# Kernel tuning notes

Hardware: AMD Instinct MI355X
Metric: run time of the kernel (lower is better)

## Reference

```python
import jax, jax.numpy as jnp
import numpy as np

B, N, D = 4, 4096, 768
K_TOP = 8  # module's self.k
EPS = 1e-12  # F.normalize eps


def setup_inputs() -> dict:
    key = jax.random.key(0)
    k0, k1, k2 = jax.random.split(key, 3)
    s = 1.0 / np.sqrt(D)
    feats = jax.random.normal(k0, (B, N, D), dtype=jnp.float32)
    Wq = jax.random.normal(k1, (D, D), dtype=jnp.float32) * s
    bq = jnp.zeros((D,), dtype=jnp.float32)
    Wkv = jax.random.normal(k2, (D, 2 * D), dtype=jnp.float32) * s
    bkv = jnp.zeros((2 * D,), dtype=jnp.float32)
    return {"feats": feats, "Wq": Wq, "bq": bq, "Wkv": Wkv, "bkv": bkv}


def _l2norm(x):
    return x / jnp.maximum(jnp.linalg.norm(x, axis=-1, keepdims=True), EPS)


def reference(feats, Wq, bq, Wkv, bkv):
    # Only self.q and self.kv are used in the original forward; the
    # transformer encoder / norm / score_head / proj are dead code there.
    b, n, d = feats.shape
    Q = feats @ Wq + bq                      # [B,N,D]
    KV = feats @ Wkv + bkv                   # [B,N,2D]
    Kmat, Vmat = jnp.split(KV, 2, axis=-1)   # [B,N,D] each

    # cosine-distance kNN graph (self excluded via +1e6 on diagonal)
    sim = jnp.einsum('bnd,bmd->bnm', _l2norm(Q), _l2norm(Kmat))
    dist = (1.0 - sim) + jnp.eye(n, dtype=sim.dtype)[None] * 1e6
    k_eff = min(n - 1, K_TOP)
    _, idx = jax.lax.top_k(-dist, k_eff)     # smallest distances -> [B,N,k]

    # gather neighbor K/V (no O(N^2 * D) expand)
    bidx = jnp.arange(b)[:, None, None]
    Kn = Kmat[bidx, idx]                     # [B,N,k,D]
    Vn = Vmat[bidx, idx]                     # [B,N,k,D]

    attn = jnp.einsum('bnd,bnkd->bnk', Q, Kn) / np.float32(np.sqrt(d))
    attn = jax.nn.softmax(attn, axis=-1)     # [B,N,k]
    out = jnp.einsum('bnk,bnkd->bnd', attn, Vn)
    return out.mean(axis=1)                  # [B,D]
```

## Files before the change

### kernel.cpp

```cpp
#include <hip/hip_runtime.h>
#include <hip/hip_bf16.h>
#include <math.h>

#define B_ 4
#define N_ 4096
#define D_ 768
#define KTOP 8
#define M_ (B_*N_)
#define TCAND 12
#define KSPLIT 16
#define QBK 32

typedef __attribute__((ext_vector_type(8))) short short8;
typedef __attribute__((ext_vector_type(4))) float f32x4;
typedef _Float16 half_t;
typedef __attribute__((ext_vector_type(8))) _Float16 half8;
typedef __attribute__((ext_vector_type(4))) _Float16 half4;

__device__ __forceinline__ ushort f2bf(float f) {
    unsigned int u = __float_as_uint(f);
    unsigned int r = (u + 0x7FFFu + ((u >> 16) & 1u)) >> 16;
    return (ushort)r;
}

__device__ __forceinline__ void gload16(const void* g, void* l) {
    __builtin_amdgcn_global_load_lds(
        (const __attribute__((address_space(1))) unsigned int*)g,
        (__attribute__((address_space(3))) unsigned int*)l, 16, 0, 0);
}

__global__ __launch_bounds__(256) void split_feats(
    const float* __restrict__ f, half_t* __restrict__ Fh, half_t* __restrict__ Fl)
{
    const int i = (blockIdx.x * 256 + threadIdx.x) * 4;
    const float4 v = *(const float4*)&f[i];
    float x[4] = {v.x, v.y, v.z, v.w};
    half4 h, l;
#pragma unroll
    for (int c = 0; c < 4; ++c) {
        const half_t hh = (half_t)x[c];
        h[c] = hh;
        l[c] = (half_t)(x[c] - (float)hh);
    }
    *(half4*)&Fh[i] = h;
    *(half4*)&Fl[i] = l;
}

__global__ __launch_bounds__(256) void split_w(
    const float* __restrict__ Wq, const float* __restrict__ Wkv,
    half_t* __restrict__ Wth, half_t* __restrict__ Wtl)
{
    __shared__ float T[64][65];
    const int tid = threadIdx.x;
    const int n0 = blockIdx.x * 64;
    const int k0 = blockIdx.y * 64;

    const int nl = tid & 63;
#pragma unroll
    for (int r = 0; r < 16; ++r) {
        const int kl = (tid >> 6) * 16 + r;
        const int n  = n0 + nl;
        const float w = (n < 768)
            ? Wq[(size_t)(k0 + kl) * 768 + n]
            : Wkv[(size_t)(k0 + kl) * 1536 + (n - 768)];
        T[kl][nl] = w;
    }
    __syncthreads();

    const int kl2 = tid & 63;
#pragma unroll
    for (int r = 0; r < 16; ++r) {
        const int nl2 = (tid >> 6) * 16 + r;
        const float ws = T[kl2][nl2] * 4096.0f;
        const half_t h = (half_t)ws;
        const half_t l = (half_t)(ws - (float)h);
        Wth[(size_t)(n0 + nl2) * D_ + k0 + kl2] = h;
        Wtl[(size_t)(n0 + nl2) * D_ + k0 + kl2] = l;
    }
}

__global__ __launch_bounds__(256) void qkv_mfma(
    const half_t* __restrict__ Fh, const half_t* __restrict__ Fl,
    const half_t* __restrict__ Wth, const half_t* __restrict__ Wtl,
    const float* __restrict__ bq, const float* __restrict__ bkv,
    float* __restrict__ Q, float* __restrict__ Km, float* __restrict__ Vm)
{
    __shared__ __align__(16) half_t Ah[128 * QBK];
    __shared__ __align__(16) half_t Al[128 * QBK];
    __shared__ __align__(16) half_t Bh[128 * QBK];
    __shared__ __align__(16) half_t Bl[128 * QBK];

    const int tid  = threadIdx.x;
    const int lane = tid & 63, w = tid >> 6;
    const int wr = w >> 1, wc = w & 1;
    const int r16 = lane & 15, kq = lane >> 4;
    const int n0 = blockIdx.x * 128;
    const int m0 = blockIdx.y * 128;
    const bool three = (n0 < 1536);

    const half_t* ah = Fh  + (size_t)(m0 + (tid >> 2)) * D_ + (tid & 3) * 8;
    const half_t* al = Fl  + (size_t)(m0 + (tid >> 2)) * D_ + (tid & 3) * 8;
    const half_t* bh = Wth + (size_t)(n0 + (tid >> 2)) * D_ + (tid & 3) * 8;
    const half_t* bl = Wtl + (size_t)(n0 + (tid >> 2)) * D_ + (tid & 3) * 8;
    half_t* lAh = Ah + (w << 9);
    half_t* lAl = Al + (w << 9);
    half_t* lBh = Bh + (w << 9);
    half_t* lBl = Bl + (w << 9);

    f32x4 acc[4][4];
#pragma unroll
    for (int mi = 0; mi < 4; ++mi)
#pragma unroll
        for (int ni = 0; ni < 4; ++ni) acc[mi][ni] = (f32x4)0.f;

    for (int kb = 0; kb < D_ / QBK; ++kb) {
#pragma unroll
        for (int i = 0; i < 2; ++i) {
            gload16(ah + (size_t)i * 64 * D_ + kb * QBK, lAh + i * 2048);
            gload16(bh + (size_t)i * 64 * D_ + kb * QBK, lBh + i * 2048);
        }
        if (three) {
#pragma unroll
            for (int i = 0; i < 2; ++i) {
                gload16(al + (size_t)i * 64 * D_ + kb * QBK, lAl + i * 2048);
                gload16(bl + (size_t)i * 64 * D_ + kb * QBK, lBl + i * 2048);
            }
        }
        __syncthreads();
        {
            half8 fa[4], fb[4];
#pragma unroll
            for (int mi = 0; mi < 4; ++mi)
                fa[mi] = *(const half8*)&Ah[(wr * 64 + mi * 16 + r16) * QBK + kq * 8];
#pragma unroll
            for (int ni = 0; ni < 4; ++ni)
                fb[ni] = *(const half8*)&Bh[(wc * 64 + ni * 16 + r16) * QBK + kq * 8];
#pragma unroll
            for (int mi = 0; mi < 4; ++mi)
#pragma unroll
                for (int ni = 0; ni < 4; ++ni)
                    acc[mi][ni] = __builtin_amdgcn_mfma_f32_16x16x32_f16(
                        fa[mi], fb[ni], acc[mi][ni], 0, 0, 0);
            if (three) {
                half8 gal[4], gbl[4];
#pragma unroll
                for (int mi = 0; mi < 4; ++mi)
                    gal[mi] = *(const half8*)&Al[(wr * 64 + mi * 16 + r16) * QBK + kq * 8];
#pragma unroll
                for (int ni = 0; ni < 4; ++ni)
                    gbl[ni] = *(const half8*)&Bl[(wc * 64 + ni * 16 + r16) * QBK + kq * 8];
#pragma unroll
                for (int mi = 0; mi < 4; ++mi)
#pragma unroll
                    for (int ni = 0; ni < 4; ++ni) {
                        acc[mi][ni] = __builtin_amdgcn_mfma_f32_16x16x32_f16(
                            fa[mi], gbl[ni], acc[mi][ni], 0, 0, 0);
                        acc[mi][ni] = __builtin_amdgcn_mfma_f32_16x16x32_f16(
                            gal[mi], fb[ni], acc[mi][ni], 0, 0, 0);
                    }
            }
        }
        __syncthreads();
    }

    const float unscale = 1.0f / 4096.0f;
#pragma unroll
    for (int ni = 0; ni < 4; ++ni) {
        const int n = n0 + wc * 64 + ni * 16 + r16;
        const float bias = (n0 < 768) ? bq[n] : bkv[n - 768];
        float* dst; int nn;
        if      (n0 < 768)  { dst = Q;  nn = n; }
        else if (n0 < 1536) { dst = Km; nn = n - 768; }
        else                { dst = Vm; nn = n - 1536; }
#pragma unroll
        for (int mi = 0; mi < 4; ++mi)
#pragma unroll
            for (int r = 0; r < 4; ++r) {
                const int m = m0 + wr * 64 + mi * 16 + kq * 4 + r;
                dst[(size_t)m * D_ + nn] = acc[mi][ni][r] * unscale + bias;
            }
    }
}

__global__ __launch_bounds__(256) void norm_bf16(
    const float* __restrict__ Q, const float* __restrict__ Km,
    ushort* __restrict__ qn, ushort* __restrict__ kn,
    float* __restrict__ rqinv, float* __restrict__ rkinv)
{
    const int wid  = blockIdx.x * 4 + (threadIdx.x >> 6);
    const int lane = threadIdx.x & 63;
    const float* src; ushort* dst; float* rv; int r;
    if (wid < M_) { src = Q;  dst = qn; rv = rqinv; r = wid; }
    else          { src = Km; dst = kn; rv = rkinv; r = wid - M_; }
    const float* p = src + (size_t)r * D_ + lane * 12;
    float v[12];
#pragma unroll
    for (int i = 0; i < 3; ++i) *(float4*)&v[i * 4] = *(const float4*)&p[i * 4];
    float s = 0.f;
#pragma unroll
    for (int i = 0; i < 12; ++i) s += v[i] * v[i];
#pragma unroll
    for (int off = 32; off; off >>= 1) s += __shfl_xor(s, off);
    const float rinv = 1.0f / fmaxf(sqrtf(s), 1e-12f);
    ushort* op = dst + (size_t)r * D_ + lane * 12;
#pragma unroll
    for (int i = 0; i < 3; ++i) {
        ushort4 o;
        o.x = f2bf(v[i * 4 + 0] * rinv); o.y = f2bf(v[i * 4 + 1] * rinv);
        o.z = f2bf(v[i * 4 + 2] * rinv); o.w = f2bf(v[i * 4 + 3] * rinv);
        *(ushort4*)&op[i * 4] = o;
    }
    if (lane == 0) rv[r] = rinv;
}

__global__ __launch_bounds__(256) void sim_gemm(
    const ushort* __restrict__ qn, const ushort* __restrict__ kn,
    ushort* __restrict__ S)
{
    __shared__ __align__(16) ushort As[128 * 64];
    __shared__ __align__(16) ushort Bs[128 * 64];

    const int tid  = threadIdx.x;
    const int lane = tid & 63, w = tid >> 6;
    const int wr = w >> 1, wc = w & 1;
    const int r16 = lane & 15, kq = lane >> 4;
    const int k0 = blockIdx.x * 128;
    const int q0 = blockIdx.y * 128;

    const ushort* qsrc = qn + (size_t)(q0 + (tid >> 3)) * D_ + (tid & 7) * 8;
    const ushort* ksrc = kn + (size_t)(k0 + (tid >> 3)) * D_ + (tid & 7) * 8;
    ushort* lA = As + ((tid >> 6) << 9);
    ushort* lB = Bs + ((tid >> 6) << 9);

    f32x4 acc[4][4];
#pragma unroll
    for (int mi = 0; mi < 4; ++mi)
#pragma unroll
        for (int ni = 0; ni < 4; ++ni) acc[mi][ni] = (f32x4)0.f;

    for (int kb = 0; kb < D_ / 64; ++kb) {
#pragma unroll
        for (int i = 0; i < 4; ++i) {
            gload16(qsrc + (size_t)i * 32 * D_ + kb * 64, lA + i * 2048);
            gload16(ksrc + (size_t)i * 32 * D_ + kb * 64, lB + i * 2048);
        }
        __syncthreads();
#pragma unroll
        for (int kk = 0; kk < 2; ++kk) {
            short8 a[4], bfr[4];
#pragma unroll
            for (int mi = 0; mi < 4; ++mi)
                a[mi] = *(const short8*)&As[(wr * 64 + mi * 16 + r16) * 64 + kk * 32 + kq * 8];
#pragma unroll
            for (int ni = 0; ni < 4; ++ni)
                bfr[ni] = *(const short8*)&Bs[(wc * 64 + ni * 16 + r16) * 64 + kk * 32 + kq * 8];
#pragma unroll
            for (int mi = 0; mi < 4; ++mi)
#pragma unroll
                for (int ni = 0; ni < 4; ++ni)
                    acc[mi][ni] = __builtin_amdgcn_mfma_f32_16x16x32_bf16(
                        a[mi], bfr[ni], acc[mi][ni], 0, 0, 0);
        }
        __syncthreads();
    }

#pragma unroll
    for (int mi = 0; mi < 4; ++mi)
#pragma unroll
        for (int ni = 0; ni < 4; ++ni)
#pragma unroll
            for (int r = 0; r < 4; ++r) {
                const int qq = q0 + wr * 64 + mi * 16 + kq * 4 + r;
                const int kk = k0 + wc * 64 + ni * 16 + r16;
                const float val = acc[mi][ni][r];
                const ushort bv = (qq == kk) ? (ushort)0xFF7Fu : f2bf(val);
                S[(size_t)qq * N_ + kk] = bv;
            }
}

__global__ __launch_bounds__(256) void sel_topk(
    const ushort* __restrict__ S, unsigned int* __restrict__ Part)
{
    const int tid = threadIdx.x;
    const int row = blockIdx.x * 256 + tid;
    const int ks  = blockIdx.y;
    const int kbase = ks * 256;
    const int KREV  = (N_ - 1) - kbase;

    const ushort* sp = S + (size_t)row * N_ + kbase;
    unsigned int t[TCAND];
#pragma unroll
    for (int i = 0; i < TCAND; ++i) t[i] = 0u;

    for (int j = 0; j < 256; j += 8) {
        const uint4 dv = *(const uint4*)(sp + j);
        unsigned int dw[4];
        dw[0] = dv.x; dw[1] = dv.y; dw[2] = dv.z; dw[3] = dv.w;
#pragma unroll
        for (int q = 0; q < 4; ++q) {
            const unsigned int vlo = dw[q] & 0xFFFFu;
            const unsigned int vhi = dw[q] >> 16;
            const unsigned int plo =
                ((vlo ^ (0x8000u + ((vlo >> 15) * 0x7FFFu))) << 16) |
                (unsigned int)(KREV - (j + 2 * q));
            const unsigned int phi =
                ((vhi ^ (0x8000u + ((vhi >> 15) * 0x7FFFu))) << 16) |
                (unsigned int)(KREV - (j + 2 * q + 1));
            unsigned int p = plo;
#pragma unroll
            for (int i = 0; i < TCAND; ++i) {
                const unsigned int mx = max(t[i], p);
                const unsigned int mn = min(t[i], p);
                t[i] = mx; p = mn;
            }
            p = phi;
#pragma unroll
            for (int i = 0; i < TCAND; ++i) {
                const unsigned int mx = max(t[i], p);
                const unsigned int mn = min(t[i], p);
                t[i] = mx; p = mn;
            }
        }
    }

    unsigned int* op = Part + (size_t)row * (KSPLIT * TCAND) + ks * TCAND;
#pragma unroll
    for (int i = 0; i < TCAND; ++i) op[i] = t[i];
}

__global__ void zero_out(float* __restrict__ out)
{
    const int i = blockIdx.x * 256 + threadIdx.x;
    if (i < B_ * D_) out[i] = 0.f;
}

__global__ __launch_bounds__(256) void merge_rescore_attn(
    const float* __restrict__ Q, const float* __restrict__ Kmat,
    const float* __restrict__ Vmat, const float* __restrict__ rqinv,
    const float* __restrict__ rkinv, const unsigned int* __restrict__ Part,
    float* __restrict__ out)
{
    __shared__ float laccum[4][D_];
    const int tid  = threadIdx.x;
    const int w    = tid >> 6, lane = tid & 63;
    const int row  = blockIdx.x * 4 + w;
    const int b    = row >> 12;

    const unsigned int* pp = Part + (size_t)row * (KSPLIT * TCAND);
    unsigned int c0 = pp[lane], c1 = pp[64 + lane], c2 = pp[128 + lane];
    unsigned int mysel = 0u;
#pragma unroll
    for (int it = 0; it < TCAND; ++it) {
        unsigned int m = max(c0, max(c1, c2));
#pragma unroll
        for (int off = 32; off; off >>= 1) m = max(m, __shfl_xor(m, off));
        c0 = (c0 == m) ? 0u : c0;
        c1 = (c1 == m) ? 0u : c1;
        c2 = (c2 == m) ? 0u : c2;
        mysel = (lane == it) ? m : mysel;
    }
    const int kj_lane = (N_ - 1) - (int)(mysel & 0xFFFFu);

    int ka[TCAND];
#pragma unroll
    for (int j = 0; j < TCAND; ++j) ka[j] = __shfl(kj_lane, j);

    float qv[12];
    {
        const float* qp = Q + (size_t)row * D_ + lane * 12;
#pragma unroll
        for (int i = 0; i < 3; ++i) *(float4*)&qv[i * 4] = *(const float4*)&qp[i * 4];
    }
    const float rq = rqinv[row];
    const float scale = 0.03608439182435161f;

    float rkl[TCAND];
#pragma unroll
    for (int j = 0; j < TCAND; ++j) rkl[j] = rkinv[(b << 12) + ka[j]];

    float d[TCAND];
#pragma unroll
    for (int j = 0; j < TCAND; ++j) d[j] = 0.f;
#pragma unroll
    for (int j = 0; j < TCAND; ++j) {
        const float* kp = Kmat + ((size_t)(b << 12) + ka[j]) * D_ + lane * 12;
#pragma unroll
        for (int i = 0; i < 3; ++i) {
            const float4 kv = *(const float4*)&kp[i * 4];
            d[j] += qv[i * 4 + 0] * kv.x + qv[i * 4 + 1] * kv.y +
                    qv[i * 4 + 2] * kv.z + qv[i * 4 + 3] * kv.w;
        }
    }
#pragma unroll
    for (int off = 32; off; off >>= 1)
#pragma unroll
        for (int j = 0; j < TCAND; ++j) d[j] += __shfl_xor(d[j], off);

    float simv[TCAND], lgv[TCAND];
#pragma unroll
    for (int j = 0; j < TCAND; ++j) {
        simv[j] = d[j] * rq * rkl[j];
        lgv[j]  = d[j] * scale;
    }

    int rk8[TCAND];
#pragma unroll
    for (int j = 0; j < TCAND; ++j) {
        int r = 0;
#pragma unroll
        for (int o = 0; o < TCAND; ++o) {
            if (o != j)
                r += (simv[o] > simv[j] ||
                      (simv[o] == simv[j] && ka[o] < ka[j])) ? 1 : 0;
        }
        rk8[j] = r;
    }

    float mx = -1e30f;
#pragma unroll
    for (int j = 0; j < TCAND; ++j) if (rk8[j] < KTOP) mx = fmaxf(mx, lgv[j]);
    float e[TCAND]; float ps = 0.f;
#pragma unroll
    for (int j = 0; j < TCAND; ++j) {
        const float ee = (rk8[j] < KTOP) ? expf(lgv[j] - mx) : 0.f;
        e[j] = ee; ps += ee;
    }
    const float inv = 1.0f / ps;

    float oacc[12];
#pragma unroll
    for (int i = 0; i < 12; ++i) oacc[i] = 0.f;
#pragma unroll
    for (int j = 0; j < TCAND; ++j) {
        if (rk8[j] < KTOP) {
            const float p = e[j] * inv;
            const float* vp = Vmat + ((size_t)(b << 12) + ka[j]) * D_ + lane * 12;
#pragma unroll
            for (int i = 0; i < 3; ++i) {
                const float4 vv = *(const float4*)&vp[i * 4];
                oacc[i * 4 + 0] += p * vv.x; oacc[i * 4 + 1] += p * vv.y;
                oacc[i * 4 + 2] += p * vv.z; oacc[i * 4 + 3] += p * vv.w;
            }
        }
    }

#pragma unroll
    for (int i = 0; i < 3; ++i)
        *(float4*)&laccum[w][lane * 12 + i * 4] = *(float4*)&oacc[i * 4];
    __syncthreads();
    for (int dd = tid; dd < D_; dd += 256) {
        const float s = laccum[0][dd] + laccum[1][dd] + laccum[2][dd] + laccum[3][dd];
        atomicAdd(&out[(size_t)b * D_ + dd], s * (1.0f / N_));
    }
}

extern "C" void kernel_launch(void* const* d_in, const int* in_sizes, int n_in,
                              void* d_out, int out_size, void* d_ws, size_t ws_size,
                              hipStream_t stream)
{
    const float* feats = (const float*)d_in[0];
    const float* Wq    = (const float*)d_in[1];
    const float* bq    = (const float*)d_in[2];
    const float* Wkv   = (const float*)d_in[3];
    const float* bkv   = (const float*)d_in[4];
    float* out = (float*)d_out;

    char* ws = (char*)d_ws;
    size_t off = 0;
    float*  Q    = (float*)(ws + off);  off += (size_t)M_ * D_ * sizeof(float);
    float*  Km   = (float*)(ws + off);  off += (size_t)M_ * D_ * sizeof(float);
    float*  Vm   = (float*)(ws + off);  off += (size_t)M_ * D_ * sizeof(float);
    char*   unio = ws + off;            off += 2 * (size_t)M_ * D_ * sizeof(ushort);
    half_t* Fh   = (half_t*)unio;
    half_t* Fl   = (half_t*)(unio + (size_t)M_ * D_ * sizeof(half_t));
    ushort* qn   = (ushort*)unio;
    ushort* kn   = (ushort*)(unio + (size_t)M_ * D_ * sizeof(ushort));
    float*  rqv  = (float*)(ws + off);  off += (size_t)M_ * sizeof(float);
    float*  rkv  = (float*)(ws + off);  off += (size_t)M_ * sizeof(float);
    half_t* Wth  = (half_t*)(ws + off); off += (size_t)2304 * D_ * sizeof(half_t);
    half_t* Wtl  = (half_t*)(ws + off); off += (size_t)2304 * D_ * sizeof(half_t);
    ushort* S    = (ushort*)(ws + off); off += (size_t)N_ * N_ * sizeof(ushort);
    unsigned int* Part = (unsigned int*)(ws + off);
    off += (size_t)M_ * KSPLIT * TCAND * sizeof(unsigned int);
    (void)ws_size; (void)in_sizes; (void)n_in; (void)out_size;

    split_feats<<<(M_ * D_) / 1024, 256, 0, stream>>>(feats, Fh, Fl);
    split_w<<<dim3(2304 / 64, D_ / 64), 256, 0, stream>>>(Wq, Wkv, Wth, Wtl);
    qkv_mfma<<<dim3(2304 / 128, M_ / 128), 256, 0, stream>>>(
        Fh, Fl, Wth, Wtl, bq, bkv, Q, Km, Vm);
    norm_bf16<<<(2 * M_) / 4, 256, 0, stream>>>(Q, Km, qn, kn, rqv, rkv);

    for (int b = 0; b < B_; ++b) {
        sim_gemm<<<dim3(N_ / 128, N_ / 128), 256, 0, stream>>>(
            qn + (size_t)b * N_ * D_, kn + (size_t)b * N_ * D_, S);
        sel_topk<<<dim3(N_ / 256, KSPLIT), 256, 0, stream>>>(
            S, Part + (size_t)b * N_ * (KSPLIT * TCAND));
    }

    zero_out<<<(B_ * D_ + 255) / 256, 256, 0, stream>>>(out);
    merge_rescore_attn<<<M_ / 4, 256, 0, stream>>>(
        Q, Km, Vm, rqv, rkv, Part, out);
}
```

Baseline: 729.2 us.

## Fuse similarity GEMM with per-tile top-k selection and widen QKV k-tile

Each similarity GEMM tile now writes its bf16 scores to shared memory and selects per-row top-12 candidates in place, so the N×N score matrix is never written to or read back from global memory. All batches run in a single 3D launch instead of a per-batch loop of two kernels. The merge kernel now reduces 32 partial candidate lists per row instead of 16, which adds work and traffic there. Separately, the QKV GEMM k-tile grows from 32 to 64, halving the number of barrier-separated iterations at the cost of doubled LDS use.

New measurement: 646.2 us. 1.13x faster.

```diff
diff --git a/kernel.cpp b/kernel.cpp
--- a/kernel.cpp
+++ b/kernel.cpp
@@ -8,8 +8,7 @@
 #define KTOP 8
 #define M_ (B_*N_)
 #define TCAND 12
-#define KSPLIT 16
-#define QBK 32
+#define SELK 32
 
 typedef __attribute__((ext_vector_type(8))) short short8;
 typedef __attribute__((ext_vector_type(4))) float f32x4;
@@ -85,10 +84,10 @@
     const float* __restrict__ bq, const float* __restrict__ bkv,
     float* __restrict__ Q, float* __restrict__ Km, float* __restrict__ Vm)
 {
-    __shared__ __align__(16) half_t Ah[128 * QBK];
-    __shared__ __align__(16) half_t Al[128 * QBK];
-    __shared__ __align__(16) half_t Bh[128 * QBK];
-    __shared__ __align__(16) half_t Bl[128 * QBK];
+    __shared__ __align__(16) half_t Ah[128 * 64];
+    __shared__ __align__(16) half_t Al[128 * 64];
+    __shared__ __align__(16) half_t Bh[128 * 64];
+    __shared__ __align__(16) half_t Bl[128 * 64];
 
     const int tid  = threadIdx.x;
     const int lane = tid & 63, w = tid >> 6;
@@ -98,10 +97,10 @@
     const int m0 = blockIdx.y * 128;
     const bool three = (n0 < 1536);
 
-    const half_t* ah = Fh  + (size_t)(m0 + (tid >> 2)) * D_ + (tid & 3) * 8;
-    const half_t* al = Fl  + (size_t)(m0 + (tid >> 2)) * D_ + (tid & 3) * 8;
-    const half_t* bh = Wth + (size_t)(n0 + (tid >> 2)) * D_ + (tid & 3) * 8;
-    const half_t* bl = Wtl + (size_t)(n0 + (tid >> 2)) * D_ + (tid & 3) * 8;
+    const half_t* ah = Fh  + (size_t)(m0 + (tid >> 3)) * D_ + (tid & 7) * 8;
+    const half_t* al = Fl  + (size_t)(m0 + (tid >> 3)) * D_ + (tid & 7) * 8;
+    const half_t* bh = Wth + (size_t)(n0 + (tid >> 3)) * D_ + (tid & 7) * 8;
+    const half_t* bl = Wtl + (size_t)(n0 + (tid >> 3)) * D_ + (tid & 7) * 8;
     half_t* lAh = Ah + (w << 9);
     half_t* lAl = Al + (w << 9);
     half_t* lBh = Bh + (w << 9);
@@ -113,28 +112,29 @@
 #pragma unroll
         for (int ni = 0; ni < 4; ++ni) acc[mi][ni] = (f32x4)0.f;
 
-    for (int kb = 0; kb < D_ / QBK; ++kb) {
-#pragma unroll
-        for (int i = 0; i < 2; ++i) {
-            gload16(ah + (size_t)i * 64 * D_ + kb * QBK, lAh + i * 2048);
-            gload16(bh + (size_t)i * 64 * D_ + kb * QBK, lBh + i * 2048);
+    for (int kb = 0; kb < D_ / 64; ++kb) {
+#pragma unroll
+        for (int i = 0; i < 4; ++i) {
+            gload16(ah + (size_t)i * 32 * D_ + kb * 64, lAh + i * 2048);
+            gload16(bh + (size_t)i * 32 * D_ + kb * 64, lBh + i * 2048);
         }
         if (three) {
 #pragma unroll
-            for (int i = 0; i < 2; ++i) {
-                gload16(al + (size_t)i * 64 * D_ + kb * QBK, lAl + i * 2048);
-                gload16(bl + (size_t)i * 64 * D_ + kb * QBK, lBl + i * 2048);
+            for (int i = 0; i < 4; ++i) {
+                gload16(al + (size_t)i * 32 * D_ + kb * 64, lAl + i * 2048);
+                gload16(bl + (size_t)i * 32 * D_ + kb * 64, lBl + i * 2048);
             }
         }
         __syncthreads();
-        {
+#pragma unroll
+        for (int kk = 0; kk < 2; ++kk) {
             half8 fa[4], fb[4];
 #pragma unroll
             for (int mi = 0; mi < 4; ++mi)
-                fa[mi] = *(const half8*)&Ah[(wr * 64 + mi * 16 + r16) * QBK + kq * 8];
+                fa[mi] = *(const half8*)&Ah[(wr * 64 + mi * 16 + r16) * 64 + kk * 32 + kq * 8];
 #pragma unroll
             for (int ni = 0; ni < 4; ++ni)
-                fb[ni] = *(const half8*)&Bh[(wc * 64 + ni * 16 + r16) * QBK + kq * 8];
+                fb[ni] = *(const half8*)&Bh[(wc * 64 + ni * 16 + r16) * 64 + kk * 32 + kq * 8];
 #pragma unroll
             for (int mi = 0; mi < 4; ++mi)
 #pragma unroll
@@ -145,10 +145,10 @@
                 half8 gal[4], gbl[4];
 #pragma unroll
                 for (int mi = 0; mi < 4; ++mi)
-                    gal[mi] = *(const half8*)&Al[(wr * 64 + mi * 16 + r16) * QBK + kq * 8];
+                    gal[mi] = *(const half8*)&Al[(wr * 64 + mi * 16 + r16) * 64 + kk * 32 + kq * 8];
 #pragma unroll
                 for (int ni = 0; ni < 4; ++ni)
-                    gbl[ni] = *(const half8*)&Bl[(wc * 64 + ni * 16 + r16) * QBK + kq * 8];
+                    gbl[ni] = *(const half8*)&Bl[(wc * 64 + ni * 16 + r16) * 64 + kk * 32 + kq * 8];
 #pragma unroll
                 for (int mi = 0; mi < 4; ++mi)
 #pragma unroll
@@ -213,12 +213,13 @@
     if (lane == 0) rv[r] = rinv;
 }
 
-__global__ __launch_bounds__(256) void sim_gemm(
-    const ushort* __restrict__ qn, const ushort* __restrict__ kn,
-    ushort* __restrict__ S)
-{
-    __shared__ __align__(16) ushort As[128 * 64];
-    __shared__ __align__(16) ushort Bs[128 * 64];
+__global__ __launch_bounds__(256) void sim_topk_fused(
+    const ushort* __restrict__ qn_all, const ushort* __restrict__ kn_all,
+    unsigned int* __restrict__ Part)
+{
+    __shared__ __align__(16) ushort smem[128 * 136];
+    ushort* As = smem;
+    ushort* Bs = smem + 128 * 64;
 
     const int tid  = threadIdx.x;
     const int lane = tid & 63, w = tid >> 6;
@@ -226,11 +227,12 @@
     const int r16 = lane & 15, kq = lane >> 4;
     const int k0 = blockIdx.x * 128;
     const int q0 = blockIdx.y * 128;
-
-    const ushort* qsrc = qn + (size_t)(q0 + (tid >> 3)) * D_ + (tid & 7) * 8;
-    const ushort* ksrc = kn + (size_t)(k0 + (tid >> 3)) * D_ + (tid & 7) * 8;
-    ushort* lA = As + ((tid >> 6) << 9);
-    ushort* lB = Bs + ((tid >> 6) << 9);
+    const int b  = blockIdx.z;
+
+    const ushort* qsrc = qn_all + ((size_t)b * N_ + q0 + (tid >> 3)) * D_ + (tid & 7) * 8;
+    const ushort* ksrc = kn_all + ((size_t)b * N_ + k0 + (tid >> 3)) * D_ + (tid & 7) * 8;
+    ushort* lA = As + (w << 9);
+    ushort* lB = Bs + (w << 9);
 
     f32x4 acc[4][4];
 #pragma unroll
@@ -264,35 +266,29 @@
         __syncthreads();
     }
 
+    ushort* St = smem;
 #pragma unroll
     for (int mi = 0; mi < 4; ++mi)
 #pragma unroll
         for (int ni = 0; ni < 4; ++ni)
 #pragma unroll
             for (int r = 0; r < 4; ++r) {
-                const int qq = q0 + wr * 64 + mi * 16 + kq * 4 + r;
-                const int kk = k0 + wc * 64 + ni * 16 + r16;
-                const float val = acc[mi][ni][r];
-                const ushort bv = (qq == kk) ? (ushort)0xFF7Fu : f2bf(val);
-                S[(size_t)qq * N_ + kk] = bv;
-            }
-}
-
-__global__ __launch_bounds__(256) void sel_topk(
-    const ushort* __restrict__ S, unsigned int* __restrict__ Part)
-{
-    const int tid = threadIdx.x;
-    const int row = blockIdx.x * 256 + tid;
-    const int ks  = blockIdx.y;
-    const int kbase = ks * 256;
-    const int KREV  = (N_ - 1) - kbase;
-
-    const ushort* sp = S + (size_t)row * N_ + kbase;
+                const int row = wr * 64 + mi * 16 + kq * 4 + r;
+                const int col = wc * 64 + ni * 16 + r16;
+                const bool diag = (q0 + row) == (k0 + col);
+                St[row * 136 + col] = diag ? (ushort)0xFF7Fu : f2bf(acc[mi][ni][r]);
+            }
+    __syncthreads();
+
+    const int rrow = tid >> 1, half = tid & 1;
+    const int KREV = (N_ - 1) - (k0 + half * 64);
+    const ushort* sp = St + rrow * 136 + half * 64;
     unsigned int t[TCAND];
 #pragma unroll
     for (int i = 0; i < TCAND; ++i) t[i] = 0u;
 
-    for (int j = 0; j < 256; j += 8) {
+#pragma unroll
+    for (int j = 0; j < 64; j += 8) {
         const uint4 dv = *(const uint4*)(sp + j);
         unsigned int dw[4];
         dw[0] = dv.x; dw[1] = dv.y; dw[2] = dv.z; dw[3] = dv.w;
@@ -322,10 +318,30 @@
             }
         }
     }
-
-    unsigned int* op = Part + (size_t)row * (KSPLIT * TCAND) + ks * TCAND;
-#pragma unroll
-    for (int i = 0; i < TCAND; ++i) op[i] = t[i];
+    __syncthreads();
+
+    unsigned int* scratch = (unsigned int*)smem;
+    if (half) {
+#pragma unroll
+        for (int i = 0; i < TCAND; ++i) scratch[rrow * TCAND + i] = t[i];
+    }
+    __syncthreads();
+    if (!half) {
+#pragma unroll
+        for (int i = 0; i < TCAND; ++i) {
+            unsigned int p = scratch[rrow * TCAND + i];
+#pragma unroll
+            for (int s = 0; s < TCAND; ++s) {
+                const unsigned int mx = max(t[s], p);
+                const unsigned int mn = min(t[s], p);
+                t[s] = mx; p = mn;
+            }
+        }
+        unsigned int* op = Part +
+            ((size_t)(b * N_ + q0 + rrow) * SELK + (k0 >> 7)) * TCAND;
+#pragma unroll
+        for (int i = 0; i < TCAND; ++i) op[i] = t[i];
+    }
 }
 
 __global__ void zero_out(float* __restrict__ out)
@@ -346,17 +362,20 @@
     const int row  = blockIdx.x * 4 + w;
     const int b    = row >> 12;
 
-    const unsigned int* pp = Part + (size_t)row * (KSPLIT * TCAND);
-    unsigned int c0 = pp[lane], c1 = pp[64 + lane], c2 = pp[128 + lane];
+    const unsigned int* pp = Part + (size_t)row * (SELK * TCAND);
+    unsigned int c[6];
+#pragma unroll
+    for (int i = 0; i < 6; ++i) c[i] = pp[i * 64 + lane];
     unsigned int mysel = 0u;
 #pragma unroll
     for (int it = 0; it < TCAND; ++it) {
-        unsigned int m = max(c0, max(c1, c2));
+        unsigned int m = c[0];
+#pragma unroll
+        for (int i = 1; i < 6; ++i) m = max(m, c[i]);
 #pragma unroll
         for (int off = 32; off; off >>= 1) m = max(m, __shfl_xor(m, off));
-        c0 = (c0 == m) ? 0u : c0;
-        c1 = (c1 == m) ? 0u : c1;
-        c2 = (c2 == m) ? 0u : c2;
+#pragma unroll
+        for (int i = 0; i < 6; ++i) c[i] = (c[i] == m) ? 0u : c[i];
         mysel = (lane == it) ? m : mysel;
     }
     const int kj_lane = (N_ - 1) - (int)(mysel & 0xFFFFu);
@@ -479,9 +498,8 @@
     float*  rkv  = (float*)(ws + off);  off += (size_t)M_ * sizeof(float);
     half_t* Wth  = (half_t*)(ws + off); off += (size_t)2304 * D_ * sizeof(half_t);
     half_t* Wtl  = (half_t*)(ws + off); off += (size_t)2304 * D_ * sizeof(half_t);
-    ushort* S    = (ushort*)(ws + off); off += (size_t)N_ * N_ * sizeof(ushort);
     unsigned int* Part = (unsigned int*)(ws + off);
-    off += (size_t)M_ * KSPLIT * TCAND * sizeof(unsigned int);
+    off += (size_t)M_ * SELK * TCAND * sizeof(unsigned int);
     (void)ws_size; (void)in_sizes; (void)n_in; (void)out_size;
 
     split_feats<<<(M_ * D_) / 1024, 256, 0, stream>>>(feats, Fh, Fl);
@@ -490,12 +508,7 @@
         Fh, Fl, Wth, Wtl, bq, bkv, Q, Km, Vm);
     norm_bf16<<<(2 * M_) / 4, 256, 0, stream>>>(Q, Km, qn, kn, rqv, rkv);
 
-    for (int b = 0; b < B_; ++b) {
-        sim_gemm<<<dim3(N_ / 128, N_ / 128), 256, 0, stream>>>(
-            qn + (size_t)b * N_ * D_, kn + (size_t)b * N_ * D_, S);
-        sel_topk<<<dim3(N_ / 256, KSPLIT), 256, 0, stream>>>(
-            S, Part + (size_t)b * N_ * (KSPLIT * TCAND));
-    }
+    sim_topk_fused<<<dim3(N_ / 128, N_ / 128, B_), 256, 0, stream>>>(qn, kn, Part);
 
     zero_out<<<(B_ * D_ + 255) / 256, 256, 0, stream>>>(out);
     merge_rescore_attn<<<M_ / 4, 256, 0, stream>>>(
```
